# Performance work log

Measured on AMD Instinct MI355X. Metric: run time of the kernel, lower is better.

## Reference

```python
import jax, jax.numpy as jnp
import numpy as np

B, S, H = 32, 2048, 512

def setup_inputs() -> dict:
    key = jax.random.key(0)
    k1, k2, k3, k4 = jax.random.split(key, 4)
    Y = jax.random.normal(k1, (B, S, H), dtype=jnp.float32)
    mask_Y = jnp.ones((B, S), dtype=jnp.float32)
    W = jax.random.normal(k2, (H, H), dtype=jnp.float32)
    b = jax.random.normal(k3, (H,), dtype=jnp.float32)
    w = jax.random.normal(k4, (H,), dtype=jnp.float32)
    return {"Y": Y, "mask_Y": mask_Y, "W": W, "b": b, "w": w}

def reference(Y, mask_Y, W, b, w):
    # u: [B,S,H] = tanh(Y @ W + b)
    u = jnp.tanh(jnp.einsum('bsh,hd->bsd', Y, W) + b)
    # scores: [B,S] = u . w, masked with large negative additive bias
    scores = jnp.einsum('bsh,h->bs', u, w) - 1000.0 * (1.0 - mask_Y)
    alpha = jax.nn.softmax(scores, axis=1)  # [B,S]
    # c_star: [B,H] = attention-weighted sum of Y
    c_star = jnp.einsum('bs,bsh->bh', alpha, Y)
    return c_star
```

## Files before the change

kernel.cpp:

```cpp
#include <hip/hip_runtime.h>
#include <hip/hip_bf16.h>


#define Bsz 32
#define Ssz 2048
#define Hsz 512
#define Msz (Bsz * Ssz)

using half8   = __attribute__((ext_vector_type(8))) _Float16;
using floatx4 = __attribute__((ext_vector_type(4))) float;

__device__ __forceinline__ void llds16(void* l, const void* g) {
  __builtin_amdgcn_global_load_lds((const __attribute__((address_space(1))) void*)g,
                                   (__attribute__((address_space(3))) void*)l, 16, 0, 0);
}

__device__ __forceinline__ float fast_tanh(float x) {
  const float e = __expf(2.f * x);
  return 1.f - 2.f / (e + 1.f);
}

__global__ __launch_bounds__(256) void wsplit_k(const float* __restrict__ W,
                                                _Float16* __restrict__ Wt) {
  __shared__ float tile[32][33];
  const int bx = blockIdx.x & 15, by = blockIdx.x >> 4;
  const int tx = threadIdx.x & 31, ty = threadIdx.x >> 5;
#pragma unroll
  for (int i = 0; i < 4; ++i)
    tile[ty + 8 * i][tx] = W[(size_t)(by * 32 + ty + 8 * i) * Hsz + bx * 32 + tx];
  __syncthreads();
#pragma unroll
  for (int i = 0; i < 4; ++i) {
    const int n = bx * 32 + ty + 8 * i;
    const int k = by * 32 + tx;
    Wt[(size_t)n * Hsz + k] = (_Float16)tile[tx][ty + 8 * i];
  }
}

__global__ __launch_bounds__(256, 3) void gemm_score_k(const float* __restrict__ Y,
                                                       const _Float16* __restrict__ Wt,
                                                       const float* __restrict__ bvec,
                                                       const float* __restrict__ wvec,
                                                       float* __restrict__ scores4) {
  __shared__ __align__(16) _Float16 Bs[128 * 32];
  const int tid = threadIdx.x;
  const int lane = tid & 63, wv = tid >> 6;
  const int lr = lane & 15, lq = lane >> 4;
  const int g = blockIdx.x;
  const int x = g & 7, q = g >> 3;
  const int nblk = q & 3;
  const int mblk = (q >> 2) * 8 + x;

  const _Float16* bW = Wt + (size_t)nblk * 128 * Hsz;

  const float* aR0 = Y + (size_t)(mblk * 128 + wv * 32 + lr) * Hsz + lq * 8;
  const float* aR1 = aR0 + (size_t)16 * Hsz;

  floatx4 acc[2][8];
#pragma unroll
  for (int rf = 0; rf < 2; ++rf)
#pragma unroll
    for (int cf = 0; cf < 8; ++cf)
      acc[rf][cf] = (floatx4){0.f, 0.f, 0.f, 0.f};

  for (int it = 0; it < 16; ++it) {
    const int k0 = it * 32;
#pragma unroll
    for (int i = 0; i < 2; ++i) {
      const int cb = i * 256 + wv * 64;
      const int p = cb + lane;
      const int row = p >> 2;
      const int gc = (p & 3) ^ ((row >> 1) & 3);
      llds16(&Bs[cb * 8], bW + (size_t)row * Hsz + k0 + gc * 8);
    }
    __syncthreads();

    const float4 f00 = *(const float4*)(aR0 + k0);
    const float4 f01 = *(const float4*)(aR0 + k0 + 4);
    const float4 f10 = *(const float4*)(aR1 + k0);
    const float4 f11 = *(const float4*)(aR1 + k0 + 4);
    half8 a0, a1;
    a0[0] = (_Float16)f00.x; a0[1] = (_Float16)f00.y;
    a0[2] = (_Float16)f00.z; a0[3] = (_Float16)f00.w;
    a0[4] = (_Float16)f01.x; a0[5] = (_Float16)f01.y;
    a0[6] = (_Float16)f01.z; a0[7] = (_Float16)f01.w;
    a1[0] = (_Float16)f10.x; a1[1] = (_Float16)f10.y;
    a1[2] = (_Float16)f10.z; a1[3] = (_Float16)f10.w;
    a1[4] = (_Float16)f11.x; a1[5] = (_Float16)f11.y;
    a1[6] = (_Float16)f11.z; a1[7] = (_Float16)f11.w;

#pragma unroll
    for (int cf = 0; cf < 8; ++cf) {
      const int nr = cf * 16 + lr;
      const half8 bf = *(const half8*)&Bs[nr * 32 + (lq ^ ((nr >> 1) & 3)) * 8];
      acc[0][cf] = __builtin_amdgcn_mfma_f32_16x16x32_f16(a0, bf, acc[0][cf], 0, 0, 0);
      acc[1][cf] = __builtin_amdgcn_mfma_f32_16x16x32_f16(a1, bf, acc[1][cf], 0, 0, 0);
    }
    __syncthreads();
  }

  float bb[8], ww[8];
#pragma unroll
  for (int cf = 0; cf < 8; ++cf) {
    const int col = nblk * 128 + cf * 16 + lr;
    bb[cf] = bvec[col];
    ww[cf] = wvec[col];
  }
#pragma unroll
  for (int rf = 0; rf < 2; ++rf) {
#pragma unroll
    for (int r = 0; r < 4; ++r) {
      float v = 0.f;
#pragma unroll
      for (int cf = 0; cf < 8; ++cf)
        v += fast_tanh(acc[rf][cf][r] + bb[cf]) * ww[cf];
      v += __shfl_xor(v, 1, 16);
      v += __shfl_xor(v, 2, 16);
      v += __shfl_xor(v, 4, 16);
      v += __shfl_xor(v, 8, 16);
      if (lr == 0)
        scores4[(size_t)nblk * Msz + mblk * 128 + wv * 32 + rf * 16 + lq * 4 + r] = v;
    }
  }
}

__global__ __launch_bounds__(256) void softmax_k(const float* __restrict__ scores4,
                                                 const float* __restrict__ mask,
                                                 float* __restrict__ alpha) {
  const int b = blockIdx.x, t = threadIdx.x;
  const int lane = t & 63, wv = t >> 6;
  float s[8];
  float mx = -3.4e38f;
#pragma unroll
  for (int i = 0; i < 8; ++i) {
    const int idx = b * Ssz + i * 256 + t;
    float v = scores4[idx] + scores4[Msz + idx] + scores4[2 * Msz + idx] + scores4[3 * Msz + idx];
    v -= 1000.f * (1.f - mask[idx]);
    s[i] = v;
    mx = fmaxf(mx, v);
  }
  for (int off = 32; off > 0; off >>= 1) mx = fmaxf(mx, __shfl_xor(mx, off, 64));
  __shared__ float rm[4], rs[4];
  if (lane == 0) rm[wv] = mx;
  __syncthreads();
  mx = fmaxf(fmaxf(rm[0], rm[1]), fmaxf(rm[2], rm[3]));
  float sum = 0.f;
#pragma unroll
  for (int i = 0; i < 8; ++i) {
    s[i] = __expf(s[i] - mx);
    sum += s[i];
  }
  for (int off = 32; off > 0; off >>= 1) sum += __shfl_xor(sum, off, 64);
  if (lane == 0) rs[wv] = sum;
  __syncthreads();
  sum = rs[0] + rs[1] + rs[2] + rs[3];
  const float inv = 1.f / sum;
#pragma unroll
  for (int i = 0; i < 8; ++i) alpha[b * Ssz + i * 256 + t] = s[i] * inv;
}

__global__ __launch_bounds__(256) void wsum1_k(const float* __restrict__ alpha,
                                               const float* __restrict__ Y,
                                               float* __restrict__ out) {
  const int b = blockIdx.x >> 5, sc = blockIdx.x & 31;
  const int t = threadIdx.x, lane = t & 63, wv = t >> 6;
  __shared__ float part[4 * 512];
  const int s0 = sc * 64 + wv * 16;
  const float* al = alpha + b * Ssz + s0;
  const float4* Yb = (const float4*)(Y + ((size_t)b * Ssz + s0) * Hsz);
  float a0 = 0.f, a1 = 0.f, a2 = 0.f, a3 = 0.f, a4 = 0.f, a5 = 0.f, a6 = 0.f, a7 = 0.f;
#pragma unroll 4
  for (int r = 0; r < 16; ++r) {
    const float a = al[r];
    const float4 y0 = Yb[r * 128 + lane * 2];
    const float4 y1 = Yb[r * 128 + lane * 2 + 1];
    a0 = fmaf(a, y0.x, a0); a1 = fmaf(a, y0.y, a1);
    a2 = fmaf(a, y0.z, a2); a3 = fmaf(a, y0.w, a3);
    a4 = fmaf(a, y1.x, a4); a5 = fmaf(a, y1.y, a5);
    a6 = fmaf(a, y1.z, a6); a7 = fmaf(a, y1.w, a7);
  }
  part[wv * 512 + 0 * 64 + lane] = a0;
  part[wv * 512 + 1 * 64 + lane] = a1;
  part[wv * 512 + 2 * 64 + lane] = a2;
  part[wv * 512 + 3 * 64 + lane] = a3;
  part[wv * 512 + 4 * 64 + lane] = a4;
  part[wv * 512 + 5 * 64 + lane] = a5;
  part[wv * 512 + 6 * 64 + lane] = a6;
  part[wv * 512 + 7 * 64 + lane] = a7;
  __syncthreads();
#pragma unroll
  for (int i = 0; i < 2; ++i) {
    const int h = i * 256 + t;
    const int idx = (h & 7) * 64 + (h >> 3);
    atomicAdd(&out[(size_t)b * Hsz + h],
              part[idx] + part[512 + idx] + part[1024 + idx] + part[1536 + idx]);
  }
}

extern "C" void kernel_launch(void* const* d_in, const int* in_sizes, int n_in,
                              void* d_out, int out_size, void* d_ws, size_t ws_size,
                              hipStream_t stream) {
  (void)in_sizes; (void)n_in; (void)out_size; (void)ws_size;
  const float* Y    = (const float*)d_in[0];
  const float* mask = (const float*)d_in[1];
  const float* W    = (const float*)d_in[2];
  const float* bvec = (const float*)d_in[3];
  const float* wvec = (const float*)d_in[4];
  float* out = (float*)d_out;

  char* ws = (char*)d_ws;
  _Float16* Wt   = (_Float16*)ws;
  float* scores4 = (float*)(ws + ((size_t)1 << 20));
  float* alpha   = (float*)(ws + ((size_t)2 << 20));

  hipMemsetAsync(out, 0, (size_t)Bsz * Hsz * sizeof(float), stream);
  wsplit_k<<<256, 256, 0, stream>>>(W, Wt);
  gemm_score_k<<<(Msz / 128) * 4, 256, 0, stream>>>(Y, Wt, bvec, wvec, scores4);
  softmax_k<<<Bsz, 256, 0, stream>>>(scores4, mask, alpha);
  wsum1_k<<<Bsz * 32, 256, 0, stream>>>(alpha, Y, out);
}
```

Baseline: 283.2 us.

## Double-buffer GEMM B tiles with prefetched A loads; fold softmax normalisation into weighted sum

The score GEMM now double-buffers the Wt tile in LDS and prefetches the next iteration's Y fragment into registers. It uses explicit vmcnt waits and raw barriers in place of full __syncthreads, so global loads overlap the MFMA work. The softmax kernel is split: a 1024-thread reduction kernel writes the combined scores plus per-batch max and inverse sum, and the weighted-sum kernel recomputes exp on the fly instead of reading a precomputed alpha. The hand-tuned waitcnt counts are fragile and depend on the compiler's load ordering, and LDS use doubles, which may affect occupancy.

After: 273.7 us. 1.03x faster.

```diff
diff --git a/kernel.cpp b/kernel.cpp
--- a/kernel.cpp
+++ b/kernel.cpp
@@ -42,7 +42,7 @@
                                                        const float* __restrict__ bvec,
                                                        const float* __restrict__ wvec,
                                                        float* __restrict__ scores4) {
-  __shared__ __align__(16) _Float16 Bs[128 * 32];
+  __shared__ __align__(16) _Float16 Bs[2][128 * 32];
   const int tid = threadIdx.x;
   const int lane = tid & 63, wv = tid >> 6;
   const int lr = lane & 15, lq = lane >> 4;
@@ -53,6 +53,17 @@
 
   const _Float16* bW = Wt + (size_t)nblk * 128 * Hsz;
 
+  int bL[2]; const _Float16* bG[2];
+#pragma unroll
+  for (int i = 0; i < 2; ++i) {
+    const int cb = i * 256 + wv * 64;
+    const int p = cb + lane;
+    const int row = p >> 2;
+    const int gc = (p & 3) ^ ((row >> 1) & 3);
+    bL[i] = cb * 8;
+    bG[i] = bW + (size_t)row * Hsz + gc * 8;
+  }
+
   const float* aR0 = Y + (size_t)(mblk * 128 + wv * 32 + lr) * Hsz + lq * 8;
   const float* aR1 = aR0 + (size_t)16 * Hsz;
 
@@ -63,22 +74,22 @@
     for (int cf = 0; cf < 8; ++cf)
       acc[rf][cf] = (floatx4){0.f, 0.f, 0.f, 0.f};
 
+#pragma unroll
+  for (int i = 0; i < 2; ++i) { llds16(&Bs[0][bL[i]], bG[i]); bG[i] += 32; }
+  __builtin_amdgcn_sched_barrier(0);
+  float4 f00 = *(const float4*)(aR0);
+  float4 f01 = *(const float4*)(aR0 + 4);
+  float4 f10 = *(const float4*)(aR1);
+  float4 f11 = *(const float4*)(aR1 + 4);
+  __builtin_amdgcn_sched_barrier(0);
+#pragma unroll
+  for (int i = 0; i < 2; ++i) { llds16(&Bs[1][bL[i]], bG[i]); bG[i] += 32; }
+
   for (int it = 0; it < 16; ++it) {
-    const int k0 = it * 32;
-#pragma unroll
-    for (int i = 0; i < 2; ++i) {
-      const int cb = i * 256 + wv * 64;
-      const int p = cb + lane;
-      const int row = p >> 2;
-      const int gc = (p & 3) ^ ((row >> 1) & 3);
-      llds16(&Bs[cb * 8], bW + (size_t)row * Hsz + k0 + gc * 8);
-    }
-    __syncthreads();
-
-    const float4 f00 = *(const float4*)(aR0 + k0);
-    const float4 f01 = *(const float4*)(aR0 + k0 + 4);
-    const float4 f10 = *(const float4*)(aR1 + k0);
-    const float4 f11 = *(const float4*)(aR1 + k0 + 4);
+    if (it < 15) asm volatile("s_waitcnt vmcnt(6)" ::: "memory");
+    else         asm volatile("s_waitcnt vmcnt(4)" ::: "memory");
+    __builtin_amdgcn_s_barrier();
+
     half8 a0, a1;
     a0[0] = (_Float16)f00.x; a0[1] = (_Float16)f00.y;
     a0[2] = (_Float16)f00.z; a0[3] = (_Float16)f00.w;
@@ -89,14 +100,29 @@
     a1[4] = (_Float16)f11.x; a1[5] = (_Float16)f11.y;
     a1[6] = (_Float16)f11.z; a1[7] = (_Float16)f11.w;
 
+    if (it < 15) {
+      const int k1 = (it + 1) * 32;
+      f00 = *(const float4*)(aR0 + k1);
+      f01 = *(const float4*)(aR0 + k1 + 4);
+      f10 = *(const float4*)(aR1 + k1);
+      f11 = *(const float4*)(aR1 + k1 + 4);
+    }
+
+    const _Float16* Bsb = Bs[it & 1];
 #pragma unroll
     for (int cf = 0; cf < 8; ++cf) {
       const int nr = cf * 16 + lr;
-      const half8 bf = *(const half8*)&Bs[nr * 32 + (lq ^ ((nr >> 1) & 3)) * 8];
+      const half8 bf = *(const half8*)&Bsb[nr * 32 + (lq ^ ((nr >> 1) & 3)) * 8];
       acc[0][cf] = __builtin_amdgcn_mfma_f32_16x16x32_f16(a0, bf, acc[0][cf], 0, 0, 0);
       acc[1][cf] = __builtin_amdgcn_mfma_f32_16x16x32_f16(a1, bf, acc[1][cf], 0, 0, 0);
     }
-    __syncthreads();
+
+    asm volatile("s_waitcnt lgkmcnt(0)" ::: "memory");
+    __builtin_amdgcn_s_barrier();
+    if (it < 14) {
+#pragma unroll
+      for (int i = 0; i < 2; ++i) { llds16(&Bs[it & 1][bL[i]], bG[i]); bG[i] += 32; }
+    }
   }
 
   float bb[8], ww[8];
@@ -124,54 +150,59 @@
   }
 }
 
-__global__ __launch_bounds__(256) void softmax_k(const float* __restrict__ scores4,
-                                                 const float* __restrict__ mask,
-                                                 float* __restrict__ alpha) {
+__global__ __launch_bounds__(1024) void red_k(const float* __restrict__ scores4,
+                                              const float* __restrict__ mask,
+                                              float* __restrict__ ssum,
+                                              float* __restrict__ minv) {
   const int b = blockIdx.x, t = threadIdx.x;
-  const int lane = t & 63, wv = t >> 6;
-  float s[8];
+  const int lane = t & 63, w = t >> 6;
+  __shared__ float rm[16], rs[16];
+  float v[2];
   float mx = -3.4e38f;
 #pragma unroll
-  for (int i = 0; i < 8; ++i) {
-    const int idx = b * Ssz + i * 256 + t;
-    float v = scores4[idx] + scores4[Msz + idx] + scores4[2 * Msz + idx] + scores4[3 * Msz + idx];
-    v -= 1000.f * (1.f - mask[idx]);
-    s[i] = v;
-    mx = fmaxf(mx, v);
+  for (int i = 0; i < 2; ++i) {
+    const int idx = b * Ssz + i * 1024 + t;
+    float s = scores4[idx] + scores4[Msz + idx] + scores4[2 * Msz + idx] + scores4[3 * Msz + idx];
+    s -= 1000.f * (1.f - mask[idx]);
+    ssum[idx] = s;
+    v[i] = s;
+    mx = fmaxf(mx, s);
   }
   for (int off = 32; off > 0; off >>= 1) mx = fmaxf(mx, __shfl_xor(mx, off, 64));
-  __shared__ float rm[4], rs[4];
-  if (lane == 0) rm[wv] = mx;
-  __syncthreads();
-  mx = fmaxf(fmaxf(rm[0], rm[1]), fmaxf(rm[2], rm[3]));
-  float sum = 0.f;
-#pragma unroll
-  for (int i = 0; i < 8; ++i) {
-    s[i] = __expf(s[i] - mx);
-    sum += s[i];
-  }
+  if (lane == 0) rm[w] = mx;
+  __syncthreads();
+  mx = rm[0];
+#pragma unroll
+  for (int i = 1; i < 16; ++i) mx = fmaxf(mx, rm[i]);
+  float sum = __expf(v[0] - mx) + __expf(v[1] - mx);
   for (int off = 32; off > 0; off >>= 1) sum += __shfl_xor(sum, off, 64);
-  if (lane == 0) rs[wv] = sum;
-  __syncthreads();
-  sum = rs[0] + rs[1] + rs[2] + rs[3];
-  const float inv = 1.f / sum;
-#pragma unroll
-  for (int i = 0; i < 8; ++i) alpha[b * Ssz + i * 256 + t] = s[i] * inv;
-}
-
-__global__ __launch_bounds__(256) void wsum1_k(const float* __restrict__ alpha,
-                                               const float* __restrict__ Y,
-                                               float* __restrict__ out) {
+  if (lane == 0) rs[w] = sum;
+  __syncthreads();
+  if (t == 0) {
+    float tot = rs[0];
+#pragma unroll
+    for (int i = 1; i < 16; ++i) tot += rs[i];
+    minv[b * 2]     = mx;
+    minv[b * 2 + 1] = 1.f / tot;
+  }
+}
+
+__global__ __launch_bounds__(256) void wsum_k(const float* __restrict__ ssum,
+                                              const float* __restrict__ minv,
+                                              const float* __restrict__ Y,
+                                              float* __restrict__ out) {
   const int b = blockIdx.x >> 5, sc = blockIdx.x & 31;
   const int t = threadIdx.x, lane = t & 63, wv = t >> 6;
   __shared__ float part[4 * 512];
   const int s0 = sc * 64 + wv * 16;
-  const float* al = alpha + b * Ssz + s0;
+  const float mx  = minv[b * 2];
+  const float inv = minv[b * 2 + 1];
+  const float* sl = ssum + b * Ssz + s0;
   const float4* Yb = (const float4*)(Y + ((size_t)b * Ssz + s0) * Hsz);
   float a0 = 0.f, a1 = 0.f, a2 = 0.f, a3 = 0.f, a4 = 0.f, a5 = 0.f, a6 = 0.f, a7 = 0.f;
 #pragma unroll 4
   for (int r = 0; r < 16; ++r) {
-    const float a = al[r];
+    const float a = __expf(sl[r] - mx) * inv;
     const float4 y0 = Yb[r * 128 + lane * 2];
     const float4 y1 = Yb[r * 128 + lane * 2 + 1];
     a0 = fmaf(a, y0.x, a0); a1 = fmaf(a, y0.y, a1);
@@ -211,11 +242,12 @@
   char* ws = (char*)d_ws;
   _Float16* Wt   = (_Float16*)ws;
   float* scores4 = (float*)(ws + ((size_t)1 << 20));
-  float* alpha   = (float*)(ws + ((size_t)2 << 20));
+  float* ssum    = (float*)(ws + ((size_t)2 << 20));
+  float* minv    = (float*)(ws + ((size_t)2304 << 10));
 
   hipMemsetAsync(out, 0, (size_t)Bsz * Hsz * sizeof(float), stream);
   wsplit_k<<<256, 256, 0, stream>>>(W, Wt);
   gemm_score_k<<<(Msz / 128) * 4, 256, 0, stream>>>(Y, Wt, bvec, wvec, scores4);
-  softmax_k<<<Bsz, 256, 0, stream>>>(scores4, mask, alpha);
-  wsum1_k<<<Bsz * 32, 256, 0, stream>>>(alpha, Y, out);
-}
+  red_k<<<Bsz, 1024, 0, stream>>>(scores4, mask, ssum, minv);
+  wsum_k<<<Bsz * 32, 256, 0, stream>>>(ssum, minv, Y, out);
+}
```
